# Optimization experiments

Measured on AMD Instinct MI355X. Metric: run time of the kernel, lower is better.

The kernel has to match this reference:

```python
import jax, jax.numpy as jnp
import numpy as np

H, W = 384, 384          # render resolution (init h, w)
TH, TW = 1024, 1024      # texture resolution
N, V, F = 2, 2048, 2048  # batch, vertices/texcoords, faces
CHUNK = 32               # faces per rasterization scan step
EPS = 1e-8


def setup_inputs() -> dict:
    key = jax.random.key(0)
    k = jax.random.split(key, 5)
    # vertices in front of camera, z ~ 3
    v = jax.random.normal(k[0], (N, V, 3), jnp.float32) * jnp.array([0.5, 0.5, 0.3], jnp.float32) + jnp.array([0.0, 0.0, 3.0], jnp.float32)
    tex = jax.random.uniform(k[1], (N, 3, TH, TW), jnp.float32)
    campos = jnp.zeros((N, 3), jnp.float32)
    camrot = jnp.broadcast_to(jnp.eye(3, dtype=jnp.float32), (N, 3, 3))
    focal = jnp.broadcast_to(400.0 * jnp.eye(2, dtype=jnp.float32), (N, 2, 2))
    princpt = jnp.broadcast_to(jnp.array([W / 2.0, H / 2.0], jnp.float32), (N, 2))
    vt = jax.random.uniform(k[2], (V, 2), jnp.float32)
    vt = vt.at[:, 1].set(1.0 - vt[:, 1])  # flip_uvs=True applied at init
    vi = jax.random.randint(k[3], (F, 3), 0, V, jnp.int32)
    vti = jax.random.randint(k[4], (F, 3), 0, V, jnp.int32)
    return {"v": v, "tex": tex, "campos": campos, "camrot": camrot, "focal": focal, "princpt": princpt, "vt": vt, "vi": vi, "vti": vti}


def _bary(x0, y0, x1, y1, x2, y2, px, py):
    # signed-area-normalized screen-space barycentrics (both windings accepted)
    area = (x1 - x0) * (y2 - y0) - (y1 - y0) * (x2 - x0)
    ok = jnp.abs(area) > 1e-9
    inv = 1.0 / jnp.where(ok, area, 1.0)
    b0 = ((x2 - x1) * (py - y1) - (y2 - y1) * (px - x1)) * inv
    b1 = ((x0 - x2) * (py - y2) - (y0 - y2) * (px - x2)) * inv
    b2 = ((x1 - x0) * (py - y0) - (y1 - y0) * (px - x0)) * inv
    return b0, b1, b2, ok


def _rasterize_one(v_pix, vi):
    # z-buffered rasterization via scan over face chunks; pixel centers at +0.5
    px = jnp.arange(W, dtype=jnp.float32)[None, None, :] + 0.5
    py = jnp.arange(H, dtype=jnp.float32)[None, :, None] + 0.5
    nch = F // CHUNK
    fids = jnp.arange(F, dtype=jnp.int32).reshape(nch, CHUNK)
    vic = vi.reshape(nch, CHUNK, 3)

    def body(carry, inp):
        zbuf, ibuf = carry
        fid, f = inp
        tri = v_pix[f]                       # [CHUNK,3,3]
        x = tri[:, :, 0][:, :, None, None]
        y = tri[:, :, 1][:, :, None, None]
        z = tri[:, :, 2][:, :, None, None]
        b0, b1, b2, ok = _bary(x[:, 0], y[:, 0], x[:, 1], y[:, 1], x[:, 2], y[:, 2], px, py)
        inside = (b0 >= 0) & (b1 >= 0) & (b2 >= 0) & ok
        zinv = b0 / z[:, 0] + b1 / z[:, 1] + b2 / z[:, 2]  # perspective-correct 1/depth
        d = jnp.where(inside & (zinv > EPS), 1.0 / jnp.maximum(zinv, EPS), jnp.inf)
        amin = jnp.argmin(d, axis=0)
        dmin = jnp.min(d, axis=0)
        upd = dmin < zbuf
        return (jnp.where(upd, dmin, zbuf), jnp.where(upd, fid[amin], ibuf)), None

    init = (jnp.full((H, W), jnp.inf, jnp.float32), jnp.full((H, W), -1, jnp.int32))
    (_, ib), _ = jax.lax.scan(body, init, (fids, vic))
    return ib


def _render_one(v_pix, vi, idx):
    # recompute perspective-correct barycentrics / depth for winning faces (differentiable)
    px = jnp.arange(W, dtype=jnp.float32)[None, :] + 0.5
    py = jnp.arange(H, dtype=jnp.float32)[:, None] + 0.5
    tri = v_pix[vi[jnp.maximum(idx, 0)]]     # [H,W,3,3]
    x, y, z = tri[..., 0], tri[..., 1], tri[..., 2]
    b0, b1, b2, ok = _bary(x[..., 0], y[..., 0], x[..., 1], y[..., 1], x[..., 2], y[..., 2], px, py)
    w0, w1, w2 = b0 / z[..., 0], b1 / z[..., 1], b2 / z[..., 2]
    zinv = jnp.maximum(w0 + w1 + w2, EPS)
    mask = idx >= 0
    depth = jnp.where(mask, 1.0 / zinv, 0.0)
    bary = jnp.where(mask[None], jnp.stack([w0, w1, w2], 0) / zinv[None], 0.0)  # [3,H,W]
    return depth, bary


def _interp_one(attr, fvi, idx, bary):
    vals = attr[fvi[jnp.maximum(idx, 0)]]    # [H,W,3,C]
    return jnp.einsum('hwkc,khw->chw', vals, bary)


def _grid_sample_one(tex, grid):
    # bilinear, align_corners=False, padding_mode='border'
    ix = ((grid[..., 0] + 1.0) * TW - 1.0) * 0.5
    iy = ((grid[..., 1] + 1.0) * TH - 1.0) * 0.5
    ix0 = jnp.floor(ix); iy0 = jnp.floor(iy)
    wx = ix - ix0; wy = iy - iy0
    x0 = jnp.clip(ix0.astype(jnp.int32), 0, TW - 1)
    x1 = jnp.clip(ix0.astype(jnp.int32) + 1, 0, TW - 1)
    y0 = jnp.clip(iy0.astype(jnp.int32), 0, TH - 1)
    y1 = jnp.clip(iy0.astype(jnp.int32) + 1, 0, TH - 1)
    g = lambda yi, xi: tex[:, yi, xi]        # [C,H,W]
    return (g(y0, x0) * (1 - wx) * (1 - wy) + g(y0, x1) * wx * (1 - wy)
            + g(y1, x0) * (1 - wx) * wy + g(y1, x1) * wx * wy)


_rasterize = jax.vmap(_rasterize_one, (0, None))
_render = jax.vmap(_render_one, (0, None, 0))
_interp = jax.vmap(_interp_one, (0, None, 0, 0))
_grid_sample = jax.vmap(_grid_sample_one)


def reference(v, tex, campos, camrot, focal, princpt, vt, vi, vti):
    # camera transform: v_cam = R (v - campos); v_pix = focal @ (xy/z) + princpt, z preserved
    v_cam = jnp.einsum('nij,nvj->nvi', camrot, v - campos[:, None, :])
    z = v_cam[..., 2:3]
    xy = jnp.einsum('nij,nvj->nvi', focal, v_cam[..., :2] / z) + princpt[:, None, :]
    v_pix = jnp.concatenate([xy, z], axis=-1)
    idx = _rasterize(jax.lax.stop_gradient(v_pix), vi)   # rasterize under no_grad
    mask = idx >= 0
    depth_img, bary_img = _render(v_pix, vi, idx)
    uv = jnp.broadcast_to(2.0 * vt - 1.0, (v.shape[0], vt.shape[0], 2))
    vt_img = _interp(uv, vti, idx, bary_img).transpose(0, 2, 3, 1)  # NHWC uv grid
    image = _grid_sample(tex, vt_img) * mask[:, None].astype(tex.dtype)
    return image
```

## Files before the change

kernel.cpp:

```cpp
#include <hip/hip_runtime.h>
#include <math.h>

#pragma clang fp contract(off)

#define NN 2
#define VV 2048
#define FF 2048
#define HH 384
#define WW 384
#define TH 1024
#define TW 1024
#define EPSD 1e-08
#define SLICES 16
#define FPS (FF / SLICES)
#define SETUP_BLOCKS ((NN * FF + 255) / 256)
#define CLEAR_BLOCKS ((NN * HH * WW + 255) / 256)

__device__ __forceinline__ float mulr(float a, float b) {
    float p = a * b;
    asm("" : "+v"(p));
    return p;
}


__global__ __launch_bounds__(256) void setup_and_clear(
    const float* __restrict__ v, const float* __restrict__ campos,
    const float* __restrict__ camrot, const float* __restrict__ focal,
    const float* __restrict__ princpt, const int* __restrict__ vi,
    const float* __restrict__ vt, const int* __restrict__ vti,
    double* __restrict__ dface, double* __restrict__ uvface,
    float4* __restrict__ cull, unsigned long long* __restrict__ keybuf)
{
#pragma clang fp contract(off)
    if (blockIdx.x >= SETUP_BLOCKS) {
        int idx = (blockIdx.x - SETUP_BLOCKS) * 256 + threadIdx.x;
        if (idx < NN * HH * WW) keybuf[idx] = 0ull;
        return;
    }
    int t = blockIdx.x * blockDim.x + threadIdx.x;
    if (t >= NN * FF) return;
    int n = t / FF, f = t % FF;
    const float* cr = camrot + n * 9;
    const float* cp = campos + n * 3;
    const float* fo = focal + n * 4;
    const float* pp = princpt + n * 2;
    float X[3], Y[3], Z[3];
    for (int k = 0; k < 3; ++k) {
        int vid = vi[f * 3 + k];
        const float* vp = v + ((size_t)n * VV + vid) * 3;
        float d0 = vp[0] - cp[0];
        float d1 = vp[1] - cp[1];
        float d2 = vp[2] - cp[2];
        float c0 = (mulr(cr[0], d0) + mulr(cr[1], d1)) + mulr(cr[2], d2);
        float c1 = (mulr(cr[3], d0) + mulr(cr[4], d1)) + mulr(cr[5], d2);
        float c2 = (mulr(cr[6], d0) + mulr(cr[7], d1)) + mulr(cr[8], d2);
        float u = c0 / c2;
        float w = c1 / c2;
        X[k] = (mulr(fo[0], u) + mulr(fo[1], w)) + pp[0];
        Y[k] = (mulr(fo[2], u) + mulr(fo[3], w)) + pp[1];
        Z[k] = c2;
    }
    float area = mulr(X[1] - X[0], Y[2] - Y[0]) - mulr(Y[1] - Y[0], X[2] - X[0]);
    bool ok = fabsf(area) > 1e-9f;
    float inv = ok ? (1.0f / area) : __builtin_nanf("");
    float e0x = X[2] - X[1], e0y = Y[2] - Y[1];
    float e1x = X[0] - X[2], e1y = Y[0] - Y[2];
    float e2x = X[1] - X[0], e2y = Y[1] - Y[0];
    double invd = (double)inv;
    double e0xd = (double)e0x, e0yd = (double)e0y;
    double e1xd = (double)e1x, e1yd = (double)e1y;
    double e2xd = (double)e2x, e2yd = (double)e2y;
    double x0d = (double)X[0], y0d = (double)Y[0];
    double x1d = (double)X[1], y1d = (double)Y[1];
    double x2d = (double)X[2], y2d = (double)Y[2];
    double rz0 = 1.0 / (double)Z[0];
    double rz1 = 1.0 / (double)Z[1];
    double rz2 = 1.0 / (double)Z[2];
    double Gx0 = -e0yd * invd, Gy0 = e0xd * invd, Gc0 = (e0yd * x1d - e0xd * y1d) * invd;
    double Gx1 = -e1yd * invd, Gy1 = e1xd * invd, Gc1 = (e1yd * x2d - e1xd * y2d) * invd;
    double Gx2 = -e2yd * invd, Gy2 = e2xd * invd, Gc2 = (e2yd * x0d - e2xd * y0d) * invd;
    double Zx = Gx0 * rz0 + Gx1 * rz1 + Gx2 * rz2;
    double Zy = Gy0 * rz0 + Gy1 * rz1 + Gy2 * rz2;
    double Zc = Gc0 * rz0 + Gc1 * rz1 + Gc2 * rz2;
    double* dd = dface + (size_t)t * 16;
    dd[0] = Gx0; dd[1] = Gy0; dd[2] = Gc0;
    dd[3] = Gx1; dd[4] = Gy1; dd[5] = Gc1;
    dd[6] = Gx2; dd[7] = Gy2; dd[8] = Gc2;
    dd[9] = Zx; dd[10] = Zy; dd[11] = Zc;
    dd[12] = 0.0; dd[13] = 0.0; dd[14] = 0.0; dd[15] = 0.0;
    int i0 = vti[f * 3 + 0], i1 = vti[f * 3 + 1], i2 = vti[f * 3 + 2];
    double u0d = (double)(2.0f * vt[i0 * 2 + 0] - 1.0f), v0d = (double)(2.0f * vt[i0 * 2 + 1] - 1.0f);
    double u1d = (double)(2.0f * vt[i1 * 2 + 0] - 1.0f), v1d = (double)(2.0f * vt[i1 * 2 + 1] - 1.0f);
    double u2d = (double)(2.0f * vt[i2 * 2 + 0] - 1.0f), v2d = (double)(2.0f * vt[i2 * 2 + 1] - 1.0f);
    double W0x = Gx0 * rz0, W0y = Gy0 * rz0, W0c = Gc0 * rz0;
    double W1x = Gx1 * rz1, W1y = Gy1 * rz1, W1c = Gc1 * rz1;
    double W2x = Gx2 * rz2, W2y = Gy2 * rz2, W2c = Gc2 * rz2;
    double* uv = uvface + (size_t)t * 8;
    uv[0] = (u0d * W0x + u1d * W1x) + u2d * W2x;
    uv[1] = (u0d * W0y + u1d * W1y) + u2d * W2y;
    uv[2] = (u0d * W0c + u1d * W1c) + u2d * W2c;
    uv[3] = (v0d * W0x + v1d * W1x) + v2d * W2x;
    uv[4] = (v0d * W0y + v1d * W1y) + v2d * W2y;
    uv[5] = (v0d * W0c + v1d * W1c) + v2d * W2c;
    uv[6] = 0.0; uv[7] = 0.0;
    float s = (area > 0.0f) ? 1.0f : -1.0f;
    float A0 = -e0y * s, B0 = e0x * s;
    float C0 = s * (float)(e0yd * x1d - e0xd * y1d);
    float A1 = -e1y * s, B1 = e1x * s;
    float C1 = s * (float)(e1yd * x2d - e1xd * y2d);
    float A2 = -e2y * s, B2 = e2x * s;
    float C2 = s * (float)(e2yd * x0d - e2xd * y0d);
    if (!ok) { C0 = -3e30f; C1 = -3e30f; C2 = -3e30f; }
    float xmn = fminf(fminf(X[0], X[1]), X[2]);
    float xmx = fmaxf(fmaxf(X[0], X[1]), X[2]);
    float ymn = fminf(fminf(Y[0], Y[1]), Y[2]);
    float ymx = fmaxf(fmaxf(Y[0], Y[1]), Y[2]);
    float4* cu = cull + (size_t)t * 4;
    cu[0] = make_float4(xmn, ymn, xmx, ymx);
    cu[1] = make_float4(A0, B0, C0, A1);
    cu[2] = make_float4(B1, C1, A2, B2);
    cu[3] = make_float4(C2, 0.0f, 0.0f, 0.0f);
}

__device__ __forceinline__ bool edge_keep(float A, float B, float C,
                                          float xlo, float xhi, float ylo, float yhi) {
    float m = A * ((A > 0.0f) ? xhi : xlo) + B * ((B > 0.0f) ? yhi : ylo) + C;
    return m >= -1.0f;
}

__global__ __launch_bounds__(256) void raster(
    const double* __restrict__ dface, const float4* __restrict__ cull,
    unsigned long long* __restrict__ keybuf)
{
#pragma clang fp contract(fast)
    __shared__ int s_cnt[4];
    __shared__ int s_list[4][FPS];
    int nz = blockIdx.z;
    int n = nz / SLICES, slice = nz % SLICES;
    int tx0 = blockIdx.x * 16, ty0 = blockIdx.y * 16;
    int tid = threadIdx.x;
    int lane = tid & 63;
    int wv = tid >> 6;
    if (tid < 4) s_cnt[tid] = 0;
    __syncthreads();
    float xlo = (float)tx0, ylo = (float)ty0;
    {
        int f = slice + (tid & 127) * SLICES;
        int qbase = (tid >> 7) * 2;
        const float4* cu = cull + ((size_t)n * FF + f) * 4;
        float4 bb = cu[0];
        if (bb.x <= xlo + 16.0f && bb.z >= xlo && bb.y <= ylo + 16.0f && bb.w >= ylo) {
            float4 c1 = cu[1], c2 = cu[2], c3 = cu[3];
            #pragma unroll
            for (int qq = 0; qq < 2; ++qq) {
                int q = qbase + qq;
                float qxlo = xlo + (float)((q & 1) * 8), qxhi = qxlo + 8.0f;
                float qylo = ylo + (float)((q >> 1) * 8), qyhi = qylo + 8.0f;
                if (bb.x <= qxhi && bb.z >= qxlo && bb.y <= qyhi && bb.w >= qylo &&
                    edge_keep(c1.x, c1.y, c1.z, qxlo, qxhi, qylo, qyhi) &&
                    edge_keep(c1.w, c2.x, c2.y, qxlo, qxhi, qylo, qyhi) &&
                    edge_keep(c2.z, c2.w, c3.x, qxlo, qxhi, qylo, qyhi)) {
                    int p = atomicAdd(&s_cnt[q], 1);
                    s_list[q][p] = f;
                }
            }
        }
    }
    __syncthreads();
    int cnt = s_cnt[wv];
    int qx0 = tx0 + (wv & 1) * 8;
    int qy0 = ty0 + (wv >> 1) * 8;
    double px = (double)(qx0 + (lane & 7)) + 0.5;
    double py = (double)(qy0 + (lane >> 3)) + 0.5;
    unsigned long long best = 0ull;
    #pragma unroll 2
    for (int i = 0; i < cnt; ++i) {
        int fid = __builtin_amdgcn_readfirstlane(s_list[wv][i]);
        const double* g = dface + ((size_t)n * FF + fid) * 16;
        double b0 = g[0] * px + (g[1] * py + g[2]);
        double b1 = g[3] * px + (g[4] * py + g[5]);
        double b2 = g[6] * px + (g[7] * py + g[8]);
        double zinv = g[9] * px + (g[10] * py + g[11]);
        if (b0 >= 0.0 && b1 >= 0.0 && b2 >= 0.0 && zinv > EPSD) {
            unsigned long long key =
                ((unsigned long long)__double_as_longlong(zinv) & ~0x7FFull)
                | (unsigned long long)(2047 - fid);
            if (key > best) best = key;
        }
    }
    if (best) {
        int x = qx0 + (lane & 7), y = qy0 + (lane >> 3);
        atomicMax(keybuf + ((size_t)n * HH + y) * WW + x, best);
    }
}

__global__ __launch_bounds__(256) void render(
    const double* __restrict__ dface, const double* __restrict__ uvface,
    const unsigned long long* __restrict__ keybuf,
    const float* __restrict__ tex, float* __restrict__ out)
{
    int t = blockIdx.x * blockDim.x + threadIdx.x;
    if (t >= NN * HH * WW) return;
    int n = t / (HH * WW);
    int p = t % (HH * WW);
    int y = p / WW, x = p % WW;
    unsigned long long k = keybuf[t];
    int f = k ? (2047 - (int)(k & 0x7FFull)) : -1;
    size_t o0 = ((size_t)(n * 3 + 0) * HH + y) * WW + x;
    size_t o1 = ((size_t)(n * 3 + 1) * HH + y) * WW + x;
    size_t o2 = ((size_t)(n * 3 + 2) * HH + y) * WW + x;
    if (f < 0) {
        out[o0] = 0.0f; out[o1] = 0.0f; out[o2] = 0.0f;
        return;
    }
    const double* g = dface + ((size_t)n * FF + f) * 16;
    const double* uv = uvface + ((size_t)n * FF + f) * 8;
    double px = (double)x + 0.5, py = (double)y + 0.5;
    double s = g[9] * px + (g[10] * py + g[11]);
    double zq = fmax(s, EPSD);
    double rzq = 1.0 / zq;
    double gx = (uv[0] * px + (uv[1] * py + uv[2])) * rzq;
    double gy = (uv[3] * px + (uv[4] * py + uv[5])) * rzq;
    double ix = ((gx + 1.0) * (double)TW - 1.0) * 0.5;
    double iy = ((gy + 1.0) * (double)TH - 1.0) * 0.5;
    double fx0 = floor(ix), fy0 = floor(iy);
    double wx = ix - fx0, wy = iy - fy0;
    int x0 = min(max((int)fx0, 0), TW - 1);
    int x1 = min(max((int)fx0 + 1, 0), TW - 1);
    int y0 = min(max((int)fy0, 0), TH - 1);
    int y1 = min(max((int)fy0 + 1, 0), TH - 1);
    double omwx = 1.0 - wx, omwy = 1.0 - wy;
    bool pair = (x1 == x0 + 1);
    #pragma unroll
    for (int c = 0; c < 3; ++c) {
        const float* tc = tex + ((size_t)n * 3 + c) * TH * TW;
        float g00, g01, g10, g11;
        if (pair) {
            float2 r0 = *(const float2*)(tc + (size_t)y0 * TW + x0);
            float2 r1 = *(const float2*)(tc + (size_t)y1 * TW + x0);
            g00 = r0.x; g01 = r0.y; g10 = r1.x; g11 = r1.y;
        } else {
            g00 = tc[(size_t)y0 * TW + x0];
            g01 = tc[(size_t)y0 * TW + x1];
            g10 = tc[(size_t)y1 * TW + x0];
            g11 = tc[(size_t)y1 * TW + x1];
        }
        double val = ((((double)g00 * omwx) * omwy + ((double)g01 * wx) * omwy)
                      + ((double)g10 * omwx) * wy) + ((double)g11 * wx) * wy;
        size_t oo = (c == 0) ? o0 : ((c == 1) ? o1 : o2);
        out[oo] = (float)val;
    }
}

extern "C" void kernel_launch(void* const* d_in, const int* in_sizes, int n_in,
                              void* d_out, int out_size, void* d_ws, size_t ws_size,
                              hipStream_t stream) {
    const float* v = (const float*)d_in[0];
    const float* tex = (const float*)d_in[1];
    const float* campos = (const float*)d_in[2];
    const float* camrot = (const float*)d_in[3];
    const float* focal = (const float*)d_in[4];
    const float* princpt = (const float*)d_in[5];
    const float* vt = (const float*)d_in[6];
    const int* vi = (const int*)d_in[7];
    const int* vti = (const int*)d_in[8];
    float* out = (float*)d_out;

    char* ws = (char*)d_ws;
    double* dface = (double*)ws;
    double* uvface = (double*)(ws + 524288);
    float4* cull = (float4*)(ws + 524288 + 262144);
    unsigned long long* keybuf =
        (unsigned long long*)(ws + 524288 + 262144 + 262144);

    setup_and_clear<<<dim3(SETUP_BLOCKS + CLEAR_BLOCKS), dim3(256), 0, stream>>>(
        v, campos, camrot, focal, princpt, vi, vt, vti, dface, uvface, cull, keybuf);
    raster<<<dim3(WW / 16, HH / 16, NN * SLICES), dim3(256), 0, stream>>>(
        dface, cull, keybuf);
    render<<<dim3((NN * HH * WW + 255) / 256), dim3(256), 0, stream>>>(
        dface, uvface, keybuf, tex, out);
}
```

Before: 147.2 us.

## Balance raster work across wavefronts via flat face-quadrant list and LDS staging

Replaces the per-quadrant face lists, where each wavefront processed only its own 8x8 quadrant, with one flat list of (quadrant, face) pairs shared by all four wavefronts. This balances the load when quadrants have uneven face counts. Face coefficients are staged cooperatively into LDS in chunks of 128, and each wave keeps four per-quadrant maxima that are merged through LDS before the atomicMax. It adds extra barriers, branchy quadrant selection and more LDS traffic in exchange for the better balance.

```diff
diff --git a/kernel.cpp b/kernel.cpp
--- a/kernel.cpp
+++ b/kernel.cpp
@@ -13,6 +13,7 @@
 #define EPSD 1e-08
 #define SLICES 16
 #define FPS (FF / SLICES)
+#define CAP 128
 #define SETUP_BLOCKS ((NN * FF + 255) / 256)
 #define CLEAR_BLOCKS ((NN * HH * WW + 255) / 256)
 
@@ -133,15 +134,16 @@
     unsigned long long* __restrict__ keybuf)
 {
 #pragma clang fp contract(fast)
-    __shared__ int s_cnt[4];
-    __shared__ int s_list[4][FPS];
+    __shared__ int s_T;
+    __shared__ int s_flat[512];
+    __shared__ double s_rec[CAP * 12];
     int nz = blockIdx.z;
     int n = nz / SLICES, slice = nz % SLICES;
     int tx0 = blockIdx.x * 16, ty0 = blockIdx.y * 16;
     int tid = threadIdx.x;
     int lane = tid & 63;
     int wv = tid >> 6;
-    if (tid < 4) s_cnt[tid] = 0;
+    if (tid == 0) s_T = 0;
     __syncthreads();
     float xlo = (float)tx0, ylo = (float)ty0;
     {
@@ -160,37 +162,70 @@
                     edge_keep(c1.x, c1.y, c1.z, qxlo, qxhi, qylo, qyhi) &&
                     edge_keep(c1.w, c2.x, c2.y, qxlo, qxhi, qylo, qyhi) &&
                     edge_keep(c2.z, c2.w, c3.x, qxlo, qxhi, qylo, qyhi)) {
-                    int p = atomicAdd(&s_cnt[q], 1);
-                    s_list[q][p] = f;
+                    int p = atomicAdd(&s_T, 1);
+                    s_flat[p] = (q << 16) | f;
                 }
             }
         }
     }
     __syncthreads();
-    int cnt = s_cnt[wv];
-    int qx0 = tx0 + (wv & 1) * 8;
-    int qy0 = ty0 + (wv >> 1) * 8;
-    double px = (double)(qx0 + (lane & 7)) + 0.5;
-    double py = (double)(qy0 + (lane >> 3)) + 0.5;
-    unsigned long long best = 0ull;
-    #pragma unroll 2
-    for (int i = 0; i < cnt; ++i) {
-        int fid = __builtin_amdgcn_readfirstlane(s_list[wv][i]);
-        const double* g = dface + ((size_t)n * FF + fid) * 16;
-        double b0 = g[0] * px + (g[1] * py + g[2]);
-        double b1 = g[3] * px + (g[4] * py + g[5]);
-        double b2 = g[6] * px + (g[7] * py + g[8]);
-        double zinv = g[9] * px + (g[10] * py + g[11]);
-        if (b0 >= 0.0 && b1 >= 0.0 && b2 >= 0.0 && zinv > EPSD) {
+    int T = s_T;
+    if (T == 0) return;
+    double pxb = (double)(tx0 + (lane & 7)) + 0.5;
+    double pyb = (double)(ty0 + (lane >> 3)) + 0.5;
+    unsigned long long best0 = 0ull, best1 = 0ull, best2 = 0ull, best3 = 0ull;
+    const double* gbase = dface + (size_t)n * FF * 16;
+    for (int base = 0; base < T; base += CAP) {
+        int cur = min(T - base, CAP);
+        for (int j = tid; j < cur * 6; j += 256) {
+            int e = j / 6;
+            int part = j - e * 6;
+            int fid = s_flat[base + e] & 0xFFFF;
+            const double2 d = *(const double2*)(gbase + (size_t)fid * 16 + part * 2);
+            *(double2*)&s_rec[e * 12 + part * 2] = d;
+        }
+        __syncthreads();
+        #pragma unroll 2
+        for (int e = wv; e < cur; e += 4) {
+            int meta = __builtin_amdgcn_readfirstlane(s_flat[base + e]);
+            int q = meta >> 16;
+            int fid = meta & 0xFFFF;
+            const double* g = &s_rec[e * 12];
+            double px = pxb + (double)((q & 1) * 8);
+            double py = pyb + (double)((q >> 1) * 8);
+            double b0 = g[0] * px + (g[1] * py + g[2]);
+            double b1 = g[3] * px + (g[4] * py + g[5]);
+            double b2 = g[6] * px + (g[7] * py + g[8]);
+            double zinv = g[9] * px + (g[10] * py + g[11]);
+            double m = fmin(fmin(b0, b1), b2);
             unsigned long long key =
                 ((unsigned long long)__double_as_longlong(zinv) & ~0x7FFull)
                 | (unsigned long long)(2047 - fid);
-            if (key > best) best = key;
+            key = (m >= 0.0 && zinv > EPSD) ? key : 0ull;
+            if (q == 0)      { if (key > best0) best0 = key; }
+            else if (q == 1) { if (key > best1) best1 = key; }
+            else if (q == 2) { if (key > best2) best2 = key; }
+            else             { if (key > best3) best3 = key; }
         }
-    }
-    if (best) {
-        int x = qx0 + (lane & 7), y = qy0 + (lane >> 3);
-        atomicMax(keybuf + ((size_t)n * HH + y) * WW + x, best);
+        __syncthreads();
+    }
+    unsigned long long* mg = (unsigned long long*)s_rec;
+    mg[(wv * 4 + 0) * 64 + lane] = best0;
+    mg[(wv * 4 + 1) * 64 + lane] = best1;
+    mg[(wv * 4 + 2) * 64 + lane] = best2;
+    mg[(wv * 4 + 3) * 64 + lane] = best3;
+    __syncthreads();
+    unsigned long long b = mg[(0 * 4 + wv) * 64 + lane];
+    unsigned long long c1 = mg[(1 * 4 + wv) * 64 + lane];
+    unsigned long long c2 = mg[(2 * 4 + wv) * 64 + lane];
+    unsigned long long c3 = mg[(3 * 4 + wv) * 64 + lane];
+    if (c1 > b) b = c1;
+    if (c2 > b) b = c2;
+    if (c3 > b) b = c3;
+    if (b) {
+        int x = tx0 + (wv & 1) * 8 + (lane & 7);
+        int y = ty0 + (wv >> 1) * 8 + (lane >> 3);
+        atomicMax(keybuf + ((size_t)n * HH + y) * WW + x, b);
     }
 }
 
```

New measurement: 157.4 us. +6.9%, slower.
